# Kernel tuning notes

Measured on AMD Instinct MI355X. Metric: run time of the kernel, lower is better.

The kernel has to match this reference:

```python
import jax, jax.numpy as jnp
import numpy as np

B, N, C, H = 128, 8732, 512, 19  # batch, priors, channels, feature map side
IMG = 300.0
FG = 19


def setup_inputs() -> dict:
    key = jax.random.key(0)
    ks = jax.random.split(key, 10)
    loc = jax.random.normal(ks[0], (B, N, 4), jnp.float32) * 0.5
    conf = jax.random.normal(ks[1], (B, N, 2), jnp.float32)
    priors = jax.random.uniform(ks[2], (N, 4), jnp.float32, minval=0.05, maxval=0.95)
    features = jax.random.normal(ks[3], (B, C, H, H), jnp.float32)
    w1 = jax.random.normal(ks[4], (C, 4096), jnp.float32) * 0.01
    b1 = jnp.zeros((4096,), jnp.float32)
    w2 = jax.random.normal(ks[5], (4096, 4096), jnp.float32) * 0.01
    b2 = jnp.zeros((4096,), jnp.float32)
    w3 = jax.random.normal(ks[6], (4096, FG), jnp.float32) * 0.01
    b3 = jnp.zeros((FG,), jnp.float32)
    return {"loc": loc, "conf": conf, "priors": priors, "features": features,
            "w1": w1, "b1": b1, "w2": w2, "b2": b2, "w3": w3, "b3": b3}


def _decode(loc, priors):
    # SSD decode, variances=[0.1, 0.2]; priors are (cx, cy, w, h)
    cxcy = priors[:, :2] + loc[..., :2] * 0.1 * priors[:, 2:]
    wh = priors[:, 2:] * jnp.exp(loc[..., 2:] * 0.2)
    xy1 = cxcy - 0.5 * wh
    return jnp.concatenate([xy1, xy1 + wh], axis=-1)  # [B,N,4] corner form


def _best_prior(loc, conf, priors):
    boxes = _decode(loc, priors)                       # [B,N,4]
    probs = jax.nn.softmax(conf, axis=-1)              # [B,N,2]
    car = jnp.argmax(probs, axis=-1) == 1              # [B,N] argmax class == car
    score = jnp.where(car, probs[..., 1], -jnp.inf)
    best = jnp.argmax(score, axis=-1)                  # [B]
    best_box = jnp.take_along_axis(boxes, best[:, None, None], axis=1)[:, 0]  # [B,4]
    has_car = jnp.any(car, axis=-1)                    # [B]
    geom = (best_box[:, 2] > best_box[:, 0]) & (best_box[:, 3] > best_box[:, 1])
    valid = has_car & geom
    result = jnp.where(has_car[:, None], best_box, 0.0)
    result = jnp.clip(result, 0.0, 1.0)
    return result, valid


def _extract(features, boxes, valid):
    # per-box crop + global max pool -> [B,C], zero for invalid boxes
    ceil_num = features.shape[2]
    step = IMG / ceil_num
    b = jnp.clip(boxes * IMG, 0.0, IMG) / step
    b = jnp.floor(jnp.clip(b, 0.0, ceil_num - 1.0)).astype(jnp.int32)  # [B,4]=x1,y1,x2,y2
    r = jnp.arange(ceil_num)
    mh = (r[None, :] >= b[:, 1:2]) & (r[None, :] <= b[:, 3:4])  # [B,H] rows
    mw = (r[None, :] >= b[:, 0:1]) & (r[None, :] <= b[:, 2:3])  # [B,W] cols
    mask = mh[:, None, :, None] & mw[:, None, None, :]          # [B,1,H,W]
    m = jnp.max(jnp.where(mask, features, -jnp.inf), axis=(2, 3))  # [B,C]
    return jnp.where(valid[:, None], m, 0.0)


def reference(loc, conf, priors, features, w1, b1, w2, b2, w3, b3):
    boxes, valid = _best_prior(loc, conf, priors)
    feat = _extract(features, boxes, valid)             # [B,512]
    h = jax.nn.relu(feat @ w1 + b1)
    h = jax.nn.relu(h @ w2 + b2)
    fg_cls = h @ w3 + b3                                # [B,19]
    return fg_cls, boxes, valid.astype(jnp.int32)
```

## Files before the change

kernel.cpp:

```cpp
#include <hip/hip_runtime.h>
#include <hip/hip_bf16.h>
#include <math.h>

#define BATCH 128
#define NPRI  8732
#define CCH   512
#define HH    19
#define NHID  4096
#define FGC   19

typedef unsigned short u16;
typedef __attribute__((ext_vector_type(8))) short bf16x8;
typedef __attribute__((ext_vector_type(4))) float f32x4;

__device__ __forceinline__ u16 f2bf(float f) {
  unsigned u = __float_as_uint(f);
  u += 0x7fff + ((u >> 16) & 1);
  return (u16)(u >> 16);
}

__global__ void k_best_partial(const float* __restrict__ conf,
                               float* __restrict__ cs, int* __restrict__ ci,
                               int* __restrict__ cc) {
  int blk = blockIdx.x;
  int b = blk >> 2, chunk = blk & 3;
  int n0 = chunk * 2183;
  int t = threadIdx.x;
  const float* cb = conf + (size_t)b * NPRI * 2;
  float bestS = -INFINITY; int bestN = 0x7fffffff; int car_any = 0;
  for (int i = n0 + t; i < n0 + 2183; i += 256) {
    float c0 = cb[2 * i], c1 = cb[2 * i + 1];
    float m = fmaxf(c0, c1);
    float e0 = expf(c0 - m), e1 = expf(c1 - m);
    float s = e0 + e1;
    float p0 = e0 / s, p1 = e1 / s;
    bool car = p1 > p0;
    car_any |= (int)car;
    float sc = car ? p1 : -INFINITY;
    if (sc > bestS || (sc == bestS && i < bestN)) { bestS = sc; bestN = i; }
  }
  __shared__ float ls[256]; __shared__ int li[256]; __shared__ int lc[256];
  ls[t] = bestS; li[t] = bestN; lc[t] = car_any;
  __syncthreads();
  for (int off = 128; off > 0; off >>= 1) {
    if (t < off) {
      float s2 = ls[t + off]; int n2 = li[t + off];
      if (s2 > ls[t] || (s2 == ls[t] && n2 < li[t])) { ls[t] = s2; li[t] = n2; }
      lc[t] |= lc[t + off];
    }
    __syncthreads();
  }
  if (t == 0) { cs[blk] = ls[0]; ci[blk] = li[0]; cc[blk] = lc[0]; }
}

__global__ void k_best_final(const float* __restrict__ loc,
                             const float* __restrict__ priors,
                             const float* __restrict__ cs,
                             const int* __restrict__ ci,
                             const int* __restrict__ cc,
                             float* __restrict__ out_boxes,
                             float* __restrict__ out_valid,
                             int4* __restrict__ crop,
                             int* __restrict__ vflag) {
  int b = threadIdx.x;
  if (b >= BATCH) return;
  float bs = -INFINITY; int bn = 0; int hc = 0;
  #pragma unroll
  for (int p = 0; p < 4; p++) {
    float s = cs[b * 4 + p]; int n = ci[b * 4 + p];
    hc |= cc[b * 4 + p];
    if (s > bs) { bs = s; bn = n; }
  }
  const float* lp = loc + ((size_t)b * NPRI + bn) * 4;
  const float* pp = priors + (size_t)bn * 4;
  float l0 = lp[0], l1 = lp[1], l2 = lp[2], l3 = lp[3];
  float pcx = pp[0], pcy = pp[1], pw = pp[2], ph = pp[3];
  float cx = pcx + (l0 * 0.1f) * pw;
  float cy = pcy + (l1 * 0.1f) * ph;
  float w = pw * expf(l2 * 0.2f);
  float h = ph * expf(l3 * 0.2f);
  float x1 = cx - 0.5f * w;
  float y1 = cy - 0.5f * h;
  float x2 = x1 + w, y2 = y1 + h;
  bool geom = (x2 > x1) && (y2 > y1);
  bool valid = hc && geom;
  float r0, r1, r2, r3;
  if (hc) { r0 = x1; r1 = y1; r2 = x2; r3 = y2; }
  else    { r0 = r1 = r2 = r3 = 0.0f; }
  r0 = fminf(fmaxf(r0, 0.0f), 1.0f);
  r1 = fminf(fmaxf(r1, 0.0f), 1.0f);
  r2 = fminf(fmaxf(r2, 0.0f), 1.0f);
  r3 = fminf(fmaxf(r3, 0.0f), 1.0f);
  out_boxes[b * 4 + 0] = r0; out_boxes[b * 4 + 1] = r1;
  out_boxes[b * 4 + 2] = r2; out_boxes[b * 4 + 3] = r3;
  out_valid[b] = valid ? 1.0f : 0.0f;
  const float stepF = (float)(300.0 / 19.0);
  float q0 = fminf(fmaxf(r0 * 300.0f, 0.0f), 300.0f) / stepF;
  float q1 = fminf(fmaxf(r1 * 300.0f, 0.0f), 300.0f) / stepF;
  float q2 = fminf(fmaxf(r2 * 300.0f, 0.0f), 300.0f) / stepF;
  float q3 = fminf(fmaxf(r3 * 300.0f, 0.0f), 300.0f) / stepF;
  int ix1 = (int)floorf(fminf(fmaxf(q0, 0.0f), 18.0f));
  int iy1 = (int)floorf(fminf(fmaxf(q1, 0.0f), 18.0f));
  int ix2 = (int)floorf(fminf(fmaxf(q2, 0.0f), 18.0f));
  int iy2 = (int)floorf(fminf(fmaxf(q3, 0.0f), 18.0f));
  crop[b] = make_int4(ix1, iy1, ix2, iy2);
  vflag[b] = valid ? 1 : 0;
}

__global__ void k_extract(const float* __restrict__ fin,
                          const int4* __restrict__ crop,
                          const int* __restrict__ vflag,
                          u16* __restrict__ feat) {
  int blk = blockIdx.x;
  int b = blk >> 7;
  int tile = blk & 127;
  int wave = threadIdx.x >> 6;
  int lane = threadIdx.x & 63;
  int c = tile * 4 + wave;
  if (!vflag[b]) {
    if (lane == 0) feat[b * CCH + c] = 0;
    return;
  }
  int4 cr = crop[b];
  int wcnt = cr.z - cr.x + 1;
  int cnt = wcnt * (cr.w - cr.y + 1);
  const float* p = fin + (size_t)(b * CCH + c) * (HH * HH);
  float m = -INFINITY;
  for (int i = lane; i < cnt; i += 64) {
    int yy = cr.y + i / wcnt;
    int xx = cr.x + i % wcnt;
    m = fmaxf(m, p[yy * HH + xx]);
  }
  #pragma unroll
  for (int off = 32; off > 0; off >>= 1) m = fmaxf(m, __shfl_xor(m, off));
  if (lane == 0) feat[b * CCH + c] = f2bf(m);
}

template <int KSPL>
__global__ __launch_bounds__(256) void k_mfma(const u16* __restrict__ A,
                                              const float* __restrict__ W,
                                              float* __restrict__ part, int K) {
  const int N = 4096;
  const int BK = 32;
  const int ST = 40;
  __shared__ u16 As[2][128 * ST];
  __shared__ u16 Bs[2][64 * ST];
  int nb = blockIdx.x;
  int ks = blockIdx.y;
  int Kper = K / KSPL;
  int k0b = ks * Kper;
  int t = threadIdx.x;
  int lane = t & 63, wave = t >> 6;
  int q = lane >> 4, r = lane & 15;

  int wm = (wave & 1) * 64;
  int wn = (wave >> 1) * 32;
  int n0 = nb * 64;

  int am = t >> 1, ah = (t & 1) * 16;
  int kp = t >> 4;
  int n4 = (t & 15) * 4;

  const u16* aptr = A + (size_t)am * K + k0b + ah;
  const float* wptr = W + (size_t)(k0b + 2 * kp) * N + n0 + n4;

  f32x4 acc[4][2];
  #pragma unroll
  for (int i = 0; i < 4; i++)
    #pragma unroll
    for (int j = 0; j < 2; j++) {
      acc[i][j].x = 0.f; acc[i][j].y = 0.f; acc[i][j].z = 0.f; acc[i][j].w = 0.f;
    }

  uint4 a0 = *(const uint4*)aptr;
  uint4 a1 = *(const uint4*)(aptr + 8);
  float4 w0 = *(const float4*)wptr;
  float4 w1 = *(const float4*)(wptr + N);
  *(uint4*)&As[0][am * ST + ah]     = a0;
  *(uint4*)&As[0][am * ST + ah + 8] = a1;
  {
    unsigned pk0 = (unsigned)f2bf(w0.x) | ((unsigned)f2bf(w1.x) << 16);
    unsigned pk1 = (unsigned)f2bf(w0.y) | ((unsigned)f2bf(w1.y) << 16);
    unsigned pk2 = (unsigned)f2bf(w0.z) | ((unsigned)f2bf(w1.z) << 16);
    unsigned pk3 = (unsigned)f2bf(w0.w) | ((unsigned)f2bf(w1.w) << 16);
    *(unsigned*)&Bs[0][(n4 + 0) * ST + 2 * kp] = pk0;
    *(unsigned*)&Bs[0][(n4 + 1) * ST + 2 * kp] = pk1;
    *(unsigned*)&Bs[0][(n4 + 2) * ST + 2 * kp] = pk2;
    *(unsigned*)&Bs[0][(n4 + 3) * ST + 2 * kp] = pk3;
  }

  const int nIter = Kper / BK;
  for (int it = 0; it < nIter; it++) {
    int cur = it & 1;
    bool more = (it + 1 < nIter);
    if (more) {
      aptr += BK;
      wptr += (size_t)BK * N;
      a0 = *(const uint4*)aptr;
      a1 = *(const uint4*)(aptr + 8);
      w0 = *(const float4*)wptr;
      w1 = *(const float4*)(wptr + N);
    }
    __syncthreads();
    bf16x8 af[4], bfr[2];
    #pragma unroll
    for (int i = 0; i < 4; i++)
      af[i] = *(const bf16x8*)&As[cur][(wm + 16 * i + r) * ST + q * 8];
    #pragma unroll
    for (int j = 0; j < 2; j++)
      bfr[j] = *(const bf16x8*)&Bs[cur][(wn + 16 * j + r) * ST + q * 8];
    #pragma unroll
    for (int i = 0; i < 4; i++)
      #pragma unroll
      for (int j = 0; j < 2; j++)
        acc[i][j] = __builtin_amdgcn_mfma_f32_16x16x32_bf16(af[i], bfr[j],
                                                            acc[i][j], 0, 0, 0);
    if (more) {
      int nxt = cur ^ 1;
      *(uint4*)&As[nxt][am * ST + ah]     = a0;
      *(uint4*)&As[nxt][am * ST + ah + 8] = a1;
      unsigned pk0 = (unsigned)f2bf(w0.x) | ((unsigned)f2bf(w1.x) << 16);
      unsigned pk1 = (unsigned)f2bf(w0.y) | ((unsigned)f2bf(w1.y) << 16);
      unsigned pk2 = (unsigned)f2bf(w0.z) | ((unsigned)f2bf(w1.z) << 16);
      unsigned pk3 = (unsigned)f2bf(w0.w) | ((unsigned)f2bf(w1.w) << 16);
      *(unsigned*)&Bs[nxt][(n4 + 0) * ST + 2 * kp] = pk0;
      *(unsigned*)&Bs[nxt][(n4 + 1) * ST + 2 * kp] = pk1;
      *(unsigned*)&Bs[nxt][(n4 + 2) * ST + 2 * kp] = pk2;
      *(unsigned*)&Bs[nxt][(n4 + 3) * ST + 2 * kp] = pk3;
    }
  }

  float* dst = part + (size_t)ks * (BATCH * N);
  #pragma unroll
  for (int i = 0; i < 4; i++)
    #pragma unroll
    for (int j = 0; j < 2; j++) {
      int col = n0 + wn + 16 * j + r;
      #pragma unroll
      for (int reg = 0; reg < 4; reg++) {
        int row = wm + 16 * i + q * 4 + reg;
        dst[(size_t)row * N + col] = acc[i][j][reg];
      }
    }
}

template <int KSPL, bool BF16OUT>
__global__ void k_finalize(const float* __restrict__ part,
                           const float* __restrict__ bias,
                           float* __restrict__ outf,
                           u16* __restrict__ outb) {
  int idx = (blockIdx.x * 256 + threadIdx.x) * 4;
  float4 s = *(const float4*)(part + idx);
  #pragma unroll
  for (int p = 1; p < KSPL; p++) {
    float4 v = *(const float4*)(part + (size_t)p * (BATCH * NHID) + idx);
    s.x += v.x; s.y += v.y; s.z += v.z; s.w += v.w;
  }
  float4 bv = *(const float4*)(bias + (idx & (NHID - 1)));
  s.x = fmaxf(s.x + bv.x, 0.0f); s.y = fmaxf(s.y + bv.y, 0.0f);
  s.z = fmaxf(s.z + bv.z, 0.0f); s.w = fmaxf(s.w + bv.w, 0.0f);
  if (BF16OUT) {
    ushort4 o;
    o.x = f2bf(s.x); o.y = f2bf(s.y); o.z = f2bf(s.z); o.w = f2bf(s.w);
    *(ushort4*)(outb + idx) = o;
  } else {
    *(float4*)(outf + idx) = s;
  }
}

__global__ void k_gemm3p(const float* __restrict__ h2,
                         const float* __restrict__ w3,
                         float* __restrict__ part3) {
  int kc = blockIdx.x;
  int t = threadIdx.x;
  __shared__ float wl[32 * FGC];
  for (int i = t; i < 32 * FGC; i += 128) wl[i] = w3[kc * 32 * FGC + i];
  __syncthreads();
  const float* hp = h2 + (size_t)t * NHID + kc * 32;
  float acc[FGC];
  #pragma unroll
  for (int j = 0; j < FGC; j++) acc[j] = 0.0f;
  for (int k = 0; k < 32; k++) {
    float hv = hp[k];
    const float* wp = &wl[k * FGC];
    #pragma unroll
    for (int j = 0; j < FGC; j++) acc[j] += hv * wp[j];
  }
  float* dst = part3 + (size_t)kc * (BATCH * FGC) + t * FGC;
  #pragma unroll
  for (int j = 0; j < FGC; j++) dst[j] = acc[j];
}

__global__ void k_fin3(const float* __restrict__ part3,
                       const float* __restrict__ b3,
                       float* __restrict__ out) {
  int j = blockIdx.x * 256 + threadIdx.x;
  if (j >= BATCH * FGC) return;
  float s = 0.0f;
  for (int p = 0; p < 128; p++) s += part3[(size_t)p * (BATCH * FGC) + j];
  out[j] = s + b3[j % FGC];
}

extern "C" void kernel_launch(void* const* d_in, const int* in_sizes, int n_in,
                              void* d_out, int out_size, void* d_ws, size_t ws_size,
                              hipStream_t stream) {
  const float* loc      = (const float*)d_in[0];
  const float* conf     = (const float*)d_in[1];
  const float* priors   = (const float*)d_in[2];
  const float* features = (const float*)d_in[3];
  const float* w1 = (const float*)d_in[4];
  const float* b1 = (const float*)d_in[5];
  const float* w2 = (const float*)d_in[6];
  const float* b2 = (const float*)d_in[7];
  const float* w3 = (const float*)d_in[8];
  const float* b3 = (const float*)d_in[9];
  float* out = (float*)d_out;

  char* ws = (char*)d_ws;
  float* part  = (float*)ws;
  float* part3 = (float*)(ws + (size_t)32 * 1024 * 1024);
  float* h2    = (float*)(ws + (size_t)34 * 1024 * 1024);
  u16*   featb = (u16*)(ws + (size_t)36 * 1024 * 1024);
  u16*   h1b   = (u16*)(ws + (size_t)36 * 1024 * 1024 + 256 * 1024);
  float* cs    = (float*)(ws + (size_t)38 * 1024 * 1024);
  int*   ci    = (int*)(cs + 512);
  int*   cc    = ci + 512;
  int4*  crop  = (int4*)(cc + 512);
  int*   vfl   = (int*)(crop + BATCH);

  k_best_partial<<<512, 256, 0, stream>>>(conf, cs, ci, cc);
  k_best_final<<<1, 128, 0, stream>>>(loc, priors, cs, ci, cc,
                                      out + BATCH * FGC,
                                      out + BATCH * FGC + BATCH * 4, crop, vfl);
  k_extract<<<BATCH * (CCH / 4), 256, 0, stream>>>(features, crop, vfl, featb);
  k_mfma<8><<<dim3(64, 8), 256, 0, stream>>>(featb, w1, part, 512);
  k_finalize<8, true><<<512, 256, 0, stream>>>(part, b1, nullptr, h1b);
  k_mfma<16><<<dim3(64, 16), 256, 0, stream>>>(h1b, w2, part, 4096);
  k_finalize<16, false><<<512, 256, 0, stream>>>(part, b2, h2, nullptr);
  k_gemm3p<<<128, 128, 0, stream>>>(h2, w3, part3);
  k_fin3<<<10, 256, 0, stream>>>(part3, b3, out);
}
```

Measured before the change: 264.6 us.

## Fuse split-K reductions, bias and ReLU into GEMM kernels and drop finalize passes

```diff
diff --git a/kernel.cpp b/kernel.cpp
--- a/kernel.cpp
+++ b/kernel.cpp
@@ -58,8 +58,8 @@
                              const float* __restrict__ cs,
                              const int* __restrict__ ci,
                              const int* __restrict__ cc,
-                             float* __restrict__ out_boxes,
-                             float* __restrict__ out_valid,
+                             const float* __restrict__ b3,
+                             float* __restrict__ out,
                              int4* __restrict__ crop,
                              int* __restrict__ vflag) {
   int b = threadIdx.x;
@@ -71,6 +71,8 @@
     hc |= cc[b * 4 + p];
     if (s > bs) { bs = s; bn = n; }
   }
+  #pragma unroll
+  for (int j = 0; j < FGC; j++) out[b * FGC + j] = b3[j];
   const float* lp = loc + ((size_t)b * NPRI + bn) * 4;
   const float* pp = priors + (size_t)bn * 4;
   float l0 = lp[0], l1 = lp[1], l2 = lp[2], l3 = lp[3];
@@ -91,9 +93,10 @@
   r1 = fminf(fmaxf(r1, 0.0f), 1.0f);
   r2 = fminf(fmaxf(r2, 0.0f), 1.0f);
   r3 = fminf(fmaxf(r3, 0.0f), 1.0f);
-  out_boxes[b * 4 + 0] = r0; out_boxes[b * 4 + 1] = r1;
-  out_boxes[b * 4 + 2] = r2; out_boxes[b * 4 + 3] = r3;
-  out_valid[b] = valid ? 1.0f : 0.0f;
+  float* ob = out + BATCH * FGC;
+  ob[b * 4 + 0] = r0; ob[b * 4 + 1] = r1;
+  ob[b * 4 + 2] = r2; ob[b * 4 + 3] = r3;
+  out[BATCH * FGC + BATCH * 4 + b] = valid ? 1.0f : 0.0f;
   const float stepF = (float)(300.0 / 19.0);
   float q0 = fminf(fmaxf(r0 * 300.0f, 0.0f), 300.0f) / stepF;
   float q1 = fminf(fmaxf(r1 * 300.0f, 0.0f), 300.0f) / stepF;
@@ -134,6 +137,91 @@
   #pragma unroll
   for (int off = 32; off > 0; off >>= 1) m = fmaxf(m, __shfl_xor(m, off));
   if (lane == 0) feat[b * CCH + c] = f2bf(m);
+}
+
+__global__ __launch_bounds__(256) void k_gemm1f(const u16* __restrict__ A,
+                                                const float* __restrict__ W,
+                                                const float* __restrict__ b1,
+                                                u16* __restrict__ h1b) {
+  const int K = 512, N = NHID, BK = 32, ST = 40;
+  __shared__ u16 As[2][128 * ST];
+  __shared__ u16 Bs[2][16 * ST];
+  int t = threadIdx.x, lane = t & 63, wave = t >> 6;
+  int q = lane >> 4, r = lane & 15;
+  int n0 = blockIdx.x * 16;
+  int wm = wave * 32;
+
+  int am = t >> 1, ah = (t & 1) * 16;
+  int kp = t >> 2, nn = (t & 3) * 4;
+
+  const u16* aptr = A + (size_t)am * K + ah;
+  const float* wptr = W + (size_t)(2 * kp) * N + n0 + nn;
+
+  f32x4 acc[2];
+  acc[0].x = acc[0].y = acc[0].z = acc[0].w = 0.f;
+  acc[1].x = acc[1].y = acc[1].z = acc[1].w = 0.f;
+
+  uint4 a0 = *(const uint4*)aptr;
+  uint4 a1 = *(const uint4*)(aptr + 8);
+  float4 w0, w1;
+  if (t < 64) { w0 = *(const float4*)wptr; w1 = *(const float4*)(wptr + N); }
+  *(uint4*)&As[0][am * ST + ah]     = a0;
+  *(uint4*)&As[0][am * ST + ah + 8] = a1;
+  if (t < 64) {
+    unsigned pk0 = (unsigned)f2bf(w0.x) | ((unsigned)f2bf(w1.x) << 16);
+    unsigned pk1 = (unsigned)f2bf(w0.y) | ((unsigned)f2bf(w1.y) << 16);
+    unsigned pk2 = (unsigned)f2bf(w0.z) | ((unsigned)f2bf(w1.z) << 16);
+    unsigned pk3 = (unsigned)f2bf(w0.w) | ((unsigned)f2bf(w1.w) << 16);
+    *(unsigned*)&Bs[0][(nn + 0) * ST + 2 * kp] = pk0;
+    *(unsigned*)&Bs[0][(nn + 1) * ST + 2 * kp] = pk1;
+    *(unsigned*)&Bs[0][(nn + 2) * ST + 2 * kp] = pk2;
+    *(unsigned*)&Bs[0][(nn + 3) * ST + 2 * kp] = pk3;
+  }
+
+  const int nIter = K / BK;
+  for (int it = 0; it < nIter; it++) {
+    int cur = it & 1;
+    bool more = (it + 1 < nIter);
+    if (more) {
+      aptr += BK;
+      wptr += (size_t)BK * N;
+      a0 = *(const uint4*)aptr;
+      a1 = *(const uint4*)(aptr + 8);
+      if (t < 64) { w0 = *(const float4*)wptr; w1 = *(const float4*)(wptr + N); }
+    }
+    __syncthreads();
+    bf16x8 af[2], bfr;
+    af[0] = *(const bf16x8*)&As[cur][(wm + r) * ST + q * 8];
+    af[1] = *(const bf16x8*)&As[cur][(wm + 16 + r) * ST + q * 8];
+    bfr   = *(const bf16x8*)&Bs[cur][r * ST + q * 8];
+    acc[0] = __builtin_amdgcn_mfma_f32_16x16x32_bf16(af[0], bfr, acc[0], 0, 0, 0);
+    acc[1] = __builtin_amdgcn_mfma_f32_16x16x32_bf16(af[1], bfr, acc[1], 0, 0, 0);
+    if (more) {
+      int nxt = cur ^ 1;
+      *(uint4*)&As[nxt][am * ST + ah]     = a0;
+      *(uint4*)&As[nxt][am * ST + ah + 8] = a1;
+      if (t < 64) {
+        unsigned pk0 = (unsigned)f2bf(w0.x) | ((unsigned)f2bf(w1.x) << 16);
+        unsigned pk1 = (unsigned)f2bf(w0.y) | ((unsigned)f2bf(w1.y) << 16);
+        unsigned pk2 = (unsigned)f2bf(w0.z) | ((unsigned)f2bf(w1.z) << 16);
+        unsigned pk3 = (unsigned)f2bf(w0.w) | ((unsigned)f2bf(w1.w) << 16);
+        *(unsigned*)&Bs[nxt][(nn + 0) * ST + 2 * kp] = pk0;
+        *(unsigned*)&Bs[nxt][(nn + 1) * ST + 2 * kp] = pk1;
+        *(unsigned*)&Bs[nxt][(nn + 2) * ST + 2 * kp] = pk2;
+        *(unsigned*)&Bs[nxt][(nn + 3) * ST + 2 * kp] = pk3;
+      }
+    }
+  }
+
+  float bv = b1[n0 + r];
+  #pragma unroll
+  for (int i = 0; i < 2; i++)
+    #pragma unroll
+    for (int reg = 0; reg < 4; reg++) {
+      int row = wm + 16 * i + q * 4 + reg;
+      float v = fmaxf(acc[i][reg] + bv, 0.0f);
+      h1b[(size_t)row * N + n0 + r] = f2bf(v);
+    }
 }
 
 template <int KSPL>
@@ -244,61 +332,66 @@
     }
 }
 
-template <int KSPL, bool BF16OUT>
-__global__ void k_finalize(const float* __restrict__ part,
-                           const float* __restrict__ bias,
-                           float* __restrict__ outf,
-                           u16* __restrict__ outb) {
-  int idx = (blockIdx.x * 256 + threadIdx.x) * 4;
-  float4 s = *(const float4*)(part + idx);
-  #pragma unroll
-  for (int p = 1; p < KSPL; p++) {
-    float4 v = *(const float4*)(part + (size_t)p * (BATCH * NHID) + idx);
-    s.x += v.x; s.y += v.y; s.z += v.z; s.w += v.w;
-  }
-  float4 bv = *(const float4*)(bias + (idx & (NHID - 1)));
-  s.x = fmaxf(s.x + bv.x, 0.0f); s.y = fmaxf(s.y + bv.y, 0.0f);
-  s.z = fmaxf(s.z + bv.z, 0.0f); s.w = fmaxf(s.w + bv.w, 0.0f);
-  if (BF16OUT) {
-    ushort4 o;
-    o.x = f2bf(s.x); o.y = f2bf(s.y); o.z = f2bf(s.z); o.w = f2bf(s.w);
-    *(ushort4*)(outb + idx) = o;
-  } else {
-    *(float4*)(outf + idx) = s;
-  }
-}
-
-__global__ void k_gemm3p(const float* __restrict__ h2,
-                         const float* __restrict__ w3,
-                         float* __restrict__ part3) {
-  int kc = blockIdx.x;
+__global__ __launch_bounds__(256) void k_gemm3f(const float* __restrict__ part,
+                                                const float* __restrict__ b2,
+                                                const float* __restrict__ w3,
+                                                float* __restrict__ out) {
+  const int KC = 128;
+  int kc = blockIdx.x, mg = blockIdx.y;
   int t = threadIdx.x;
-  __shared__ float wl[32 * FGC];
-  for (int i = t; i < 32 * FGC; i += 128) wl[i] = w3[kc * 32 * FGC + i];
+  __shared__ float wl[KC * FGC];
+  __shared__ float red[256][FGC];
+  for (int i = t; i < KC * FGC; i += 256) wl[i] = w3[kc * KC * FGC + i];
   __syncthreads();
-  const float* hp = h2 + (size_t)t * NHID + kc * 32;
+  int mrow = t >> 3, sub = t & 7;
+  int m = mg * 32 + mrow;
+  int kk0 = sub * 16;
+  int kg = kc * KC + kk0;
+  float4 s[4];
+  #pragma unroll
+  for (int v = 0; v < 4; v++)
+    s[v] = *(const float4*)(part + (size_t)m * NHID + kg + 4 * v);
+  #pragma unroll
+  for (int p = 1; p < 8; p++) {
+    const float* pp = part + (size_t)p * (BATCH * NHID) + (size_t)m * NHID + kg;
+    #pragma unroll
+    for (int v = 0; v < 4; v++) {
+      float4 x = *(const float4*)(pp + 4 * v);
+      s[v].x += x.x; s[v].y += x.y; s[v].z += x.z; s[v].w += x.w;
+    }
+  }
   float acc[FGC];
   #pragma unroll
   for (int j = 0; j < FGC; j++) acc[j] = 0.0f;
-  for (int k = 0; k < 32; k++) {
-    float hv = hp[k];
-    const float* wp = &wl[k * FGC];
-    #pragma unroll
-    for (int j = 0; j < FGC; j++) acc[j] += hv * wp[j];
-  }
-  float* dst = part3 + (size_t)kc * (BATCH * FGC) + t * FGC;
-  #pragma unroll
-  for (int j = 0; j < FGC; j++) dst[j] = acc[j];
-}
-
-__global__ void k_fin3(const float* __restrict__ part3,
-                       const float* __restrict__ b3,
-                       float* __restrict__ out) {
-  int j = blockIdx.x * 256 + threadIdx.x;
-  if (j >= BATCH * FGC) return;
-  float s = 0.0f;
-  for (int p = 0; p < 128; p++) s += part3[(size_t)p * (BATCH * FGC) + j];
-  out[j] = s + b3[j % FGC];
+  #pragma unroll
+  for (int v = 0; v < 4; v++) {
+    float4 bv = *(const float4*)(b2 + kg + 4 * v);
+    float h[4];
+    h[0] = fmaxf(s[v].x + bv.x, 0.0f);
+    h[1] = fmaxf(s[v].y + bv.y, 0.0f);
+    h[2] = fmaxf(s[v].z + bv.z, 0.0f);
+    h[3] = fmaxf(s[v].w + bv.w, 0.0f);
+    #pragma unroll
+    for (int e = 0; e < 4; e++) {
+      const float* wp = &wl[(kk0 + 4 * v + e) * FGC];
+      #pragma unroll
+      for (int j = 0; j < FGC; j++) acc[j] += h[e] * wp[j];
+    }
+  }
+  #pragma unroll
+  for (int j = 0; j < FGC; j++) red[t][j] = acc[j];
+  __syncthreads();
+  for (int off = 4; off > 0; off >>= 1) {
+    if (sub < off) {
+      #pragma unroll
+      for (int j = 0; j < FGC; j++) red[t][j] += red[t + off][j];
+    }
+    __syncthreads();
+  }
+  if (sub == 0) {
+    #pragma unroll
+    for (int j = 0; j < FGC; j++) atomicAdd(&out[m * FGC + j], red[t][j]);
+  }
 }
 
 extern "C" void kernel_launch(void* const* d_in, const int* in_sizes, int n_in,
@@ -318,25 +411,19 @@
 
   char* ws = (char*)d_ws;
   float* part  = (float*)ws;
-  float* part3 = (float*)(ws + (size_t)32 * 1024 * 1024);
-  float* h2    = (float*)(ws + (size_t)34 * 1024 * 1024);
-  u16*   featb = (u16*)(ws + (size_t)36 * 1024 * 1024);
-  u16*   h1b   = (u16*)(ws + (size_t)36 * 1024 * 1024 + 256 * 1024);
-  float* cs    = (float*)(ws + (size_t)38 * 1024 * 1024);
+  u16*   featb = (u16*)(ws + (size_t)16 * 1024 * 1024);
+  u16*   h1b   = (u16*)(ws + (size_t)17 * 1024 * 1024);
+  float* cs    = (float*)(ws + (size_t)18 * 1024 * 1024);
   int*   ci    = (int*)(cs + 512);
   int*   cc    = ci + 512;
   int4*  crop  = (int4*)(cc + 512);
   int*   vfl   = (int*)(crop + BATCH);
 
   k_best_partial<<<512, 256, 0, stream>>>(conf, cs, ci, cc);
-  k_best_final<<<1, 128, 0, stream>>>(loc, priors, cs, ci, cc,
-                                      out + BATCH * FGC,
-                                      out + BATCH * FGC + BATCH * 4, crop, vfl);
+  k_best_final<<<1, 128, 0, stream>>>(loc, priors, cs, ci, cc, b3,
+                                      out, crop, vfl);
   k_extract<<<BATCH * (CCH / 4), 256, 0, stream>>>(features, crop, vfl, featb);
-  k_mfma<8><<<dim3(64, 8), 256, 0, stream>>>(featb, w1, part, 512);
-  k_finalize<8, true><<<512, 256, 0, stream>>>(part, b1, nullptr, h1b);
-  k_mfma<16><<<dim3(64, 16), 256, 0, stream>>>(h1b, w2, part, 4096);
-  k_finalize<16, false><<<512, 256, 0, stream>>>(part, b2, h2, nullptr);
-  k_gemm3p<<<128, 128, 0, stream>>>(h2, w3, part3);
-  k_fin3<<<10, 256, 0, stream>>>(part3, b3, out);
-}
+  k_gemm1f<<<256, 256, 0, stream>>>(featb, w1, b1, h1b);
+  k_mfma<8><<<dim3(64, 8), 256, 0, stream>>>(h1b, w2, part, 4096);
+  k_gemm3f<<<dim3(32, 4), 256, 0, stream>>>(part, b2, w3, out);
+}
```

Result: slower. 272.5 us (+3.0%).
